# Performance work log

Measured on AMD Instinct MI355X. Metric: run time of the kernel, lower is better.

The kernel has to match this reference:

```python
import jax, jax.numpy as jnp
import numpy as np

D_MODEL = 1024
N_HEADS = 16
D_K = D_MODEL // N_HEADS
BATCH = 4
SEQ = 2048


def setup_inputs() -> dict:
    key = jax.random.key(0)
    ks = jax.random.split(key, 12)
    s = 1.0 / np.sqrt(D_MODEL)
    inp = {
        "context_sequence": jax.random.normal(ks[0], (BATCH, SEQ, D_MODEL), jnp.float32),
        "value_sequence": jax.random.normal(ks[1], (BATCH, SEQ, D_MODEL), jnp.float32),
        # True = masked (causal: cannot attend to future positions)
        "mask": jnp.triu(jnp.ones((SEQ, SEQ), dtype=bool), k=1),
        "Wq": jax.random.uniform(ks[2], (D_MODEL, D_MODEL), jnp.float32, -s, s),
        "bq": jax.random.uniform(ks[3], (D_MODEL,), jnp.float32, -s, s),
        "Wk": jax.random.uniform(ks[4], (D_MODEL, D_MODEL), jnp.float32, -s, s),
        "bk": jax.random.uniform(ks[5], (D_MODEL,), jnp.float32, -s, s),
        "Wv": jax.random.uniform(ks[6], (D_MODEL, D_MODEL), jnp.float32, -s, s),
        "bv": jax.random.uniform(ks[7], (D_MODEL,), jnp.float32, -s, s),
        "Wo": jax.random.uniform(ks[8], (D_MODEL, D_MODEL), jnp.float32, -s, s),
        "bo": jax.random.uniform(ks[9], (D_MODEL,), jnp.float32, -s, s),
    }
    return inp


def reference(context_sequence, value_sequence, mask, Wq, bq, Wk, bk, Wv, bv, Wo, bo):
    B, S, _ = context_sequence.shape
    # projections; split heads: [B, H, S, Dk]
    def split_heads(x):
        return x.reshape(B, S, N_HEADS, D_K).transpose(0, 2, 1, 3)

    Q = split_heads(context_sequence @ Wq + bq)
    K = split_heads(context_sequence @ Wk + bk)
    V = split_heads(value_sequence @ Wv + bv)

    scale = 1.0 / jnp.sqrt(jnp.asarray(D_K, dtype=Q.dtype))
    scores = jnp.einsum("bhqd,bhkd->bhqk", Q, K) * scale  # [B,H,S,S]
    scores = jnp.where(mask, jnp.asarray(-1e9, dtype=scores.dtype), scores)
    attn = jax.nn.softmax(scores, axis=-1)
    out = jnp.einsum("bhqk,bhkd->bhqd", attn, V)
    out = out.transpose(0, 2, 1, 3).reshape(B, S, D_MODEL)
    return out @ Wo + bo  # dropout p=0 (eval) -> identity
```

## Files before the change

kernel.cpp:

```cpp
#include <hip/hip_runtime.h>
#include <stdint.h>

#define D_MODEL 1024
#define SEQ 2048
#define BATCH 4
#define NH 16
#define DK 64

typedef float f32x4 __attribute__((ext_vector_type(4)));
typedef float f32x16 __attribute__((ext_vector_type(16)));
typedef __bf16 bf16x8 __attribute__((ext_vector_type(8)));
typedef unsigned short us4v __attribute__((ext_vector_type(4)));

__device__ __forceinline__ unsigned short f2bf(float f) {
  union { float f; unsigned u; } x; x.f = f;
  unsigned r = x.u + 0x7FFFu + ((x.u >> 16) & 1u);
  return (unsigned short)(r >> 16);
}

__device__ __forceinline__ void gll16(const void* g, void* l) {
  __builtin_amdgcn_global_load_lds(
      (__attribute__((address_space(1))) void*)g,
      (__attribute__((address_space(3))) void*)l, 16, 0, 0);
}

__device__ __forceinline__ int cvtpk(float lo, float hi) {
  int r;
  asm("v_cvt_pk_bf16_f32 %0, %1, %2" : "=v"(r) : "v"(lo), "v"(hi));
  return r;
}
__device__ __forceinline__ void pl32swap(int& a, int& b) {
  asm volatile("v_permlane32_swap_b32 %0, %1" : "+v"(a), "+v"(b));
}
__device__ __forceinline__ float exp2fast(float x) {
  float r;
  asm("v_exp_f32 %0, %1" : "=v"(r) : "v"(x));
  return r;
}

__global__ void cvtbf2(const float* __restrict__ a, const float* __restrict__ b,
                       unsigned short* __restrict__ out, const int nseg) {
  const int t = blockIdx.x * blockDim.x + threadIdx.x;
  const int stride = gridDim.x * blockDim.x;
  for (int i = t * 4; i < 2 * nseg; i += stride * 4) {
    const float* src = (i < nseg) ? &a[i] : &b[i - nseg];
    const float4 v = *(const float4*)src;
    us4v o;
    o[0] = f2bf(v.x); o[1] = f2bf(v.y); o[2] = f2bf(v.z); o[3] = f2bf(v.w);
    *(us4v*)&out[i] = o;
  }
}

__global__ void wtrans(const float* __restrict__ W0, const float* __restrict__ W1,
                       const float* __restrict__ W2, const float* __restrict__ W3,
                       unsigned short* __restrict__ T0, unsigned short* __restrict__ T1,
                       unsigned short* __restrict__ T2, unsigned short* __restrict__ T3) {
  __shared__ float t[32][33];
  const int z = blockIdx.z;
  const float* W = (z == 0) ? W0 : (z == 1) ? W1 : (z == 2) ? W2 : W3;
  unsigned short* T = (z == 0) ? T0 : (z == 1) ? T1 : (z == 2) ? T2 : T3;
  const int n0 = blockIdx.x * 32, k0 = blockIdx.y * 32;
  const int tx = threadIdx.x, ty = threadIdx.y;
#pragma unroll
  for (int i = 0; i < 4; ++i)
    t[ty + 8 * i][tx] = W[(size_t)(k0 + ty + 8 * i) * D_MODEL + n0 + tx];
  __syncthreads();
#pragma unroll
  for (int i = 0; i < 4; ++i)
    T[(size_t)(n0 + ty + 8 * i) * D_MODEL + k0 + tx] = f2bf(t[tx][ty + 8 * i]);
}

__global__ __launch_bounds__(256) void gemm128(
    const unsigned short* __restrict__ A, const unsigned short* __restrict__ Bt,
    const float* __restrict__ bias, unsigned short* __restrict__ outb,
    float* __restrict__ outf, const int mode) {
  __shared__ __align__(16) unsigned short Alds[2 * 128 * 64];
  __shared__ __align__(16) unsigned short Blds[2 * 128 * 64];
  const int tid = threadIdx.x;
  const int lane = tid & 63;
  const int w = tid >> 6;
  const int wr = w >> 1, wc = w & 1;

  int flat = (int)blockIdx.x + 8 * (int)blockIdx.y;
  flat = (flat & 7) * 64 + (flat >> 3);
  const int n0 = (flat & 7) * 128;
  const int m0 = (flat >> 3) * 128;

  const int srow = tid >> 3, sslot = tid & 7;

  auto stage = [&](int kk, int buf) {
#pragma unroll
    for (int i = 0; i < 4; ++i) {
      const int r = srow + 32 * i;
      const int gc = kk * 64 + ((sslot ^ (r & 7)) << 3);
      gll16(A + (size_t)(m0 + r) * D_MODEL + gc, &Alds[buf * 8192 + tid * 8 + i * 2048]);
      gll16(Bt + (size_t)(n0 + r) * D_MODEL + gc, &Blds[buf * 8192 + tid * 8 + i * 2048]);
    }
  };

  f32x4 acc[4][4] = {};

  stage(0, 0);
  stage(1, 1);

  const int NK = D_MODEL / 64;
  for (int kk = 0; kk < NK; ++kk) {
    const int cur = kk & 1;
    if (kk + 1 < NK) asm volatile("s_waitcnt vmcnt(8)" ::: "memory");
    else             asm volatile("s_waitcnt vmcnt(0)" ::: "memory");
    __builtin_amdgcn_s_barrier();
    asm volatile("" ::: "memory");

    const unsigned short* Al = &Alds[cur * 8192];
    const unsigned short* Bl = &Blds[cur * 8192];
#pragma unroll
    for (int kf = 0; kf < 2; ++kf) {
      const int sb = kf * 4 + (lane >> 4);
      bf16x8 a[4], b[4];
#pragma unroll
      for (int m = 0; m < 4; ++m) {
        const int row = wr * 64 + m * 16 + (lane & 15);
        a[m] = *(const bf16x8*)&Al[row * 64 + ((sb ^ (row & 7)) << 3)];
      }
#pragma unroll
      for (int n = 0; n < 4; ++n) {
        const int row = wc * 64 + n * 16 + (lane & 15);
        b[n] = *(const bf16x8*)&Bl[row * 64 + ((sb ^ (row & 7)) << 3)];
      }
#pragma unroll
      for (int m = 0; m < 4; ++m)
#pragma unroll
        for (int n = 0; n < 4; ++n)
          acc[m][n] = __builtin_amdgcn_mfma_f32_16x16x32_bf16(a[m], b[n], acc[m][n], 0, 0, 0);
    }

    asm volatile("" ::: "memory");
    __builtin_amdgcn_s_barrier();

    if (kk + 2 < NK) stage(kk + 2, cur);
  }

#pragma unroll
  for (int m = 0; m < 4; ++m) {
    const int rb = m0 + wr * 64 + m * 16 + ((lane >> 4) << 2);
#pragma unroll
    for (int n = 0; n < 4; ++n) {
      const int col = n0 + wc * 64 + n * 16 + (lane & 15);
      const float bv = bias[col];
#pragma unroll
      for (int j = 0; j < 4; ++j) {
        const int row = rb + j;
        const float v = acc[m][n][j] + bv;
        if (mode == 2) {
          outf[(size_t)row * D_MODEL + col] = v;
        } else {
          const int b_ = row >> 11, s_ = row & (SEQ - 1);
          const int h_ = col >> 6, d_ = col & (DK - 1);
          size_t idx;
          if (mode == 0) idx = (((size_t)(b_ * NH + h_)) * SEQ + s_) * DK + d_;
          else           idx = (((size_t)(b_ * NH + h_)) * DK + d_) * SEQ + s_;
          outb[idx] = f2bf(v);
        }
      }
    }
  }
}

__global__ __launch_bounds__(256, 4) void attn4w(
    const unsigned short* __restrict__ Q, const unsigned short* __restrict__ K,
    const unsigned short* __restrict__ Vt, unsigned short* __restrict__ O) {
  __shared__ __align__(16) unsigned short Klds[2 * 64 * 64];
  __shared__ __align__(16) unsigned short Vlds[2 * 64 * 64];

  const int tid = threadIdx.x, lane = tid & 63, w = tid >> 6;
  const int lq = lane & 31, hi = lane >> 5;
  const int bh = blockIdx.x;
  const int strip = 15 - (int)blockIdx.y;
  const size_t qkbase = (size_t)bh * SEQ * DK;
  const size_t vbase = (size_t)bh * DK * SEQ;
  const int srow = tid >> 3, sslot = tid & 7;
  const int b_ = bh >> 4, h_ = bh & (NH - 1);

  const int q0 = strip * 128;
  const int qw0 = q0 + w * 32;
  const int qg = qw0 + lq;
  const int n = 2 * strip + 2;

  bf16x8 qb[4];
  {
    const float QSCALE = 0.125f * 1.44269504f;
    const unsigned short* qp = Q + qkbase + (size_t)qg * DK + hi * 8;
#pragma unroll
    for (int ks = 0; ks < 4; ++ks) {
      qb[ks] = *(const bf16x8*)(qp + ks * 16);
#pragma unroll
      for (int e = 0; e < 8; ++e)
        qb[ks][e] = (__bf16)((float)qb[ks][e] * QSCALE);
    }
  }

  float m = -3e38f, l = 0.f;
  f32x16 o0 = {}, o1 = {};

#pragma unroll
  for (int i = 0; i < 2; ++i) {
    const int r = srow + 32 * i;
    const int sc = (sslot ^ (r & 7)) << 3;
    gll16(K + qkbase + (size_t)r * DK + sc, &Klds[tid * 8 + i * 2048]);
    gll16(Vt + vbase + (size_t)r * SEQ + sc, &Vlds[tid * 8 + i * 2048]);
  }
#pragma unroll
  for (int i = 0; i < 2; ++i) {
    const int r = srow + 32 * i;
    const int sc = (sslot ^ (r & 7)) << 3;
    gll16(K + qkbase + (size_t)(64 + r) * DK + sc, &Klds[4096 + tid * 8 + i * 2048]);
    gll16(Vt + vbase + (size_t)r * SEQ + 64 + sc, &Vlds[4096 + tid * 8 + i * 2048]);
  }

  for (int jt = 0; jt < n; ++jt) {
    const int cur = jt & 1;
    if (jt + 1 < n) asm volatile("s_waitcnt vmcnt(4)" ::: "memory");
    else            asm volatile("s_waitcnt vmcnt(0)" ::: "memory");
    __builtin_amdgcn_s_barrier();
    asm volatile("" ::: "memory");

    if (64 * jt < qw0 + 32) {
      const unsigned short* Kl = &Klds[cur * 4096];
      const unsigned short* Vl = &Vlds[cur * 4096];

      f32x16 st0 = {}, st1 = {};
      __builtin_amdgcn_s_setprio(1);
#pragma unroll
      for (int ks = 0; ks < 4; ++ks) {
        const int so = ((ks * 2 + hi) ^ (lq & 7)) << 3;
        const bf16x8 ka0 = *(const bf16x8*)&Kl[lq * 64 + so];
        const bf16x8 ka1 = *(const bf16x8*)&Kl[(32 + lq) * 64 + so];
        st0 = __builtin_amdgcn_mfma_f32_32x32x16_bf16(ka0, qb[ks], st0, 0, 0, 0);
        st1 = __builtin_amdgcn_mfma_f32_32x32x16_bf16(ka1, qb[ks], st1, 0, 0, 0);
      }
      __builtin_amdgcn_s_setprio(0);

      if (64 * jt + 63 > qw0) {
        const int rb = 64 * jt + 4 * hi - qg;
#pragma unroll
        for (int r = 0; r < 16; ++r) {
          const int crow0 = (r & 3) + 8 * (r >> 2);
          if (crow0 + rb > 0)      st0[r] = -3e38f;
          if (crow0 + 32 + rb > 0) st1[r] = -3e38f;
        }
      }

      float tmax[8];
#pragma unroll
      for (int r = 0; r < 8; ++r)
        tmax[r] = fmaxf(fmaxf(st0[r], st0[r + 8]), fmaxf(st1[r], st1[r + 8]));
      float mx = fmaxf(fmaxf(fmaxf(tmax[0], tmax[1]), fmaxf(tmax[2], tmax[3])),
                       fmaxf(fmaxf(tmax[4], tmax[5]), fmaxf(tmax[6], tmax[7])));
      mx = fmaxf(mx, __shfl_xor(mx, 32));

      if (__any((int)(mx > m + 11.5416f))) {
        const float mnew = fmaxf(m, mx);
        const float alpha = exp2fast(m - mnew);
        m = mnew;
        l *= alpha;
#pragma unroll
        for (int r = 0; r < 16; ++r) { o0[r] *= alpha; o1[r] *= alpha; }
      }

#pragma unroll
      for (int r = 0; r < 16; ++r) {
        st0[r] = exp2fast(st0[r] - m);
        st1[r] = exp2fast(st1[r] - m);
      }

      float tsum[8];
#pragma unroll
      for (int r = 0; r < 8; ++r)
        tsum[r] = (st0[r] + st0[r + 8]) + (st1[r] + st1[r + 8]);
      float rs = ((tsum[0] + tsum[1]) + (tsum[2] + tsum[3])) +
                 ((tsum[4] + tsum[5]) + (tsum[6] + tsum[7]));
      rs += __shfl_xor(rs, 32);
      l += rs;

      bf16x8 pb[4];
#pragma unroll
      for (int ks = 0; ks < 4; ++ks) {
        const int base = (ks & 1) * 8;
        float p0, p1, p2, p3, p4, p5, p6, p7;
        if (ks < 2) {
          p0 = st0[base + 0]; p1 = st0[base + 1]; p2 = st0[base + 2]; p3 = st0[base + 3];
          p4 = st0[base + 4]; p5 = st0[base + 5]; p6 = st0[base + 6]; p7 = st0[base + 7];
        } else {
          p0 = st1[base + 0]; p1 = st1[base + 1]; p2 = st1[base + 2]; p3 = st1[base + 3];
          p4 = st1[base + 4]; p5 = st1[base + 5]; p6 = st1[base + 6]; p7 = st1[base + 7];
        }
        int a0 = cvtpk(p0, p1), a1 = cvtpk(p2, p3);
        int a2 = cvtpk(p4, p5), a3 = cvtpk(p6, p7);
        pl32swap(a0, a2);
        pl32swap(a1, a3);
        union { int i[4]; bf16x8 v; } u;
        u.i[0] = a0; u.i[1] = a1; u.i[2] = a2; u.i[3] = a3;
        pb[ks] = u.v;
      }

      __builtin_amdgcn_s_setprio(1);
#pragma unroll
      for (int ks = 0; ks < 4; ++ks) {
        const int so = ((ks * 2 + hi) ^ (lq & 7)) << 3;
        const bf16x8 va0 = *(const bf16x8*)&Vl[lq * 64 + so];
        const bf16x8 va1 = *(const bf16x8*)&Vl[(32 + lq) * 64 + so];
        o0 = __builtin_amdgcn_mfma_f32_32x32x16_bf16(va0, pb[ks], o0, 0, 0, 0);
        o1 = __builtin_amdgcn_mfma_f32_32x32x16_bf16(va1, pb[ks], o1, 0, 0, 0);
      }
      __builtin_amdgcn_s_setprio(0);
    }

    asm volatile("" ::: "memory");
    __builtin_amdgcn_s_barrier();

    if (jt + 2 < n) {
      const int kv0 = (jt + 2) * 64;
#pragma unroll
      for (int i = 0; i < 2; ++i) {
        const int r = srow + 32 * i;
        const int sc = (sslot ^ (r & 7)) << 3;
        gll16(K + qkbase + (size_t)(kv0 + r) * DK + sc,
              &Klds[cur * 4096 + tid * 8 + i * 2048]);
        gll16(Vt + vbase + (size_t)r * SEQ + kv0 + sc,
              &Vlds[cur * 4096 + tid * 8 + i * 2048]);
      }
    }
  }

  const float rl = 1.0f / l;
  unsigned short* orow = O + (size_t)(b_ * SEQ + qg) * D_MODEL + h_ * DK;
#pragma unroll
  for (int g = 0; g < 4; ++g) {
    us4v pk0, pk1;
#pragma unroll
    for (int j = 0; j < 4; ++j) {
      pk0[j] = f2bf(o0[4 * g + j] * rl);
      pk1[j] = f2bf(o1[4 * g + j] * rl);
    }
    const int d0 = 8 * g + 4 * hi;
    *(us4v*)&orow[d0] = pk0;
    *(us4v*)&orow[32 + d0] = pk1;
  }
}

extern "C" void kernel_launch(void* const* d_in, const int* in_sizes, int n_in,
                              void* d_out, int out_size, void* d_ws, size_t ws_size,
                              hipStream_t stream) {
  const float* ctx = (const float*)d_in[0];
  const float* val = (const float*)d_in[1];
  const float* Wq = (const float*)d_in[3];
  const float* bq = (const float*)d_in[4];
  const float* Wk = (const float*)d_in[5];
  const float* bk = (const float*)d_in[6];
  const float* Wv = (const float*)d_in[7];
  const float* bv = (const float*)d_in[8];
  const float* Wo = (const float*)d_in[9];
  const float* bo = (const float*)d_in[10];

  unsigned short* ws = (unsigned short*)d_ws;
  const size_t XSZ = (size_t)BATCH * SEQ * D_MODEL;
  const size_t WSZ = (size_t)D_MODEL * D_MODEL;
  unsigned short* Xc  = ws;
  unsigned short* Xv  = Xc + XSZ;
  unsigned short* Wqt = Xv + XSZ;
  unsigned short* Wkt = Wqt + WSZ;
  unsigned short* Wvt = Wkt + WSZ;
  unsigned short* Wot = Wvt + WSZ;
  unsigned short* Qb  = Wot + WSZ;
  unsigned short* Kb  = Qb + XSZ;
  unsigned short* Vtb = Kb + XSZ;
  unsigned short* Ob  = Vtb + XSZ;

  cvtbf2<<<2048, 256, 0, stream>>>(ctx, val, Xc, (int)XSZ);
  wtrans<<<dim3(32, 32, 4), dim3(32, 8), 0, stream>>>(Wq, Wk, Wv, Wo, Wqt, Wkt, Wvt, Wot);

  dim3 gg(D_MODEL / 128, BATCH * SEQ / 128);
  gemm128<<<gg, 256, 0, stream>>>(Xc, Wqt, bq, Qb, nullptr, 0);
  gemm128<<<gg, 256, 0, stream>>>(Xc, Wkt, bk, Kb, nullptr, 0);
  gemm128<<<gg, 256, 0, stream>>>(Xv, Wvt, bv, Vtb, nullptr, 1);

  attn4w<<<dim3(BATCH * NH, 16), 256, 0, stream>>>(Qb, Kb, Vtb, Ob);

  gemm128<<<gg, 256, 0, stream>>>(Ob, Wot, bo, nullptr, (float*)d_out, 2);
}
```

Before: 180.1 us.

## Batch QKV GEMMs into one launch and triple-buffer attention K/V loads

The three Q/K/V projection GEMMs become one launch using blockIdx.z to pick operands, which removes two launches and lets their tails overlap. In the attention kernel, K/V staging moves to a three-slot LDS ring issued right after the barrier, so the second barrier per iteration is dropped and prefetch starts earlier. The row-sum cross-half shuffle is deferred to after the loop, and the max reduction now uses permlane32_swap instead of a shuffle. Occupancy hint drops from 4 to 3 blocks per CU because LDS use grows by half.

```diff
diff --git a/kernel.cpp b/kernel.cpp
--- a/kernel.cpp
+++ b/kernel.cpp
@@ -31,6 +31,12 @@
 }
 __device__ __forceinline__ void pl32swap(int& a, int& b) {
   asm volatile("v_permlane32_swap_b32 %0, %1" : "+v"(a), "+v"(b));
+}
+__device__ __forceinline__ float xmax32(float x) {
+  int a = __float_as_int(x), b;
+  asm volatile("v_mov_b32 %0, %1" : "=v"(b) : "v"(a));
+  pl32swap(a, b);
+  return fmaxf(__int_as_float(a), __int_as_float(b));
 }
 __device__ __forceinline__ float exp2fast(float x) {
   float r;
@@ -70,12 +76,11 @@
     T[(size_t)(n0 + ty + 8 * i) * D_MODEL + k0 + tx] = f2bf(t[tx][ty + 8 * i]);
 }
 
-__global__ __launch_bounds__(256) void gemm128(
+__device__ __forceinline__ void gemm_body(
     const unsigned short* __restrict__ A, const unsigned short* __restrict__ Bt,
     const float* __restrict__ bias, unsigned short* __restrict__ outb,
-    float* __restrict__ outf, const int mode) {
-  __shared__ __align__(16) unsigned short Alds[2 * 128 * 64];
-  __shared__ __align__(16) unsigned short Blds[2 * 128 * 64];
+    float* __restrict__ outf, const int mode,
+    unsigned short* Alds, unsigned short* Blds) {
   const int tid = threadIdx.x;
   const int lane = tid & 63;
   const int w = tid >> 6;
@@ -166,11 +171,37 @@
   }
 }
 
-__global__ __launch_bounds__(256, 4) void attn4w(
+__global__ __launch_bounds__(256) void gemmQKV(
+    const unsigned short* __restrict__ Xc, const unsigned short* __restrict__ Xv,
+    const unsigned short* __restrict__ Wqt, const unsigned short* __restrict__ Wkt,
+    const unsigned short* __restrict__ Wvt,
+    const float* __restrict__ bq, const float* __restrict__ bk,
+    const float* __restrict__ bv,
+    unsigned short* __restrict__ Qb, unsigned short* __restrict__ Kb,
+    unsigned short* __restrict__ Vtb) {
+  __shared__ __align__(16) unsigned short Alds[2 * 128 * 64];
+  __shared__ __align__(16) unsigned short Blds[2 * 128 * 64];
+  const int z = blockIdx.z;
+  const unsigned short* A = (z == 2) ? Xv : Xc;
+  const unsigned short* Bt = (z == 0) ? Wqt : (z == 1) ? Wkt : Wvt;
+  const float* bias = (z == 0) ? bq : (z == 1) ? bk : bv;
+  unsigned short* outb = (z == 0) ? Qb : (z == 1) ? Kb : Vtb;
+  gemm_body(A, Bt, bias, outb, nullptr, (z == 2) ? 1 : 0, Alds, Blds);
+}
+
+__global__ __launch_bounds__(256) void gemmO(
+    const unsigned short* __restrict__ A, const unsigned short* __restrict__ Bt,
+    const float* __restrict__ bias, float* __restrict__ outf) {
+  __shared__ __align__(16) unsigned short Alds[2 * 128 * 64];
+  __shared__ __align__(16) unsigned short Blds[2 * 128 * 64];
+  gemm_body(A, Bt, bias, nullptr, outf, 2, Alds, Blds);
+}
+
+__global__ __launch_bounds__(256, 3) void attn4w(
     const unsigned short* __restrict__ Q, const unsigned short* __restrict__ K,
     const unsigned short* __restrict__ Vt, unsigned short* __restrict__ O) {
-  __shared__ __align__(16) unsigned short Klds[2 * 64 * 64];
-  __shared__ __align__(16) unsigned short Vlds[2 * 64 * 64];
+  __shared__ __align__(16) unsigned short Klds[3 * 64 * 64];
+  __shared__ __align__(16) unsigned short Vlds[3 * 64 * 64];
 
   const int tid = threadIdx.x, lane = tid & 63, w = tid >> 6;
   const int lq = lane & 31, hi = lane >> 5;
@@ -186,6 +217,18 @@
   const int qg = qw0 + lq;
   const int n = 2 * strip + 2;
 
+  auto stageKV = [&](int t, int slot) {
+#pragma unroll
+    for (int i = 0; i < 2; ++i) {
+      const int r = srow + 32 * i;
+      const int sc = (sslot ^ (r & 7)) << 3;
+      gll16(K + qkbase + (size_t)(t * 64 + r) * DK + sc,
+            &Klds[slot * 4096 + tid * 8 + i * 2048]);
+      gll16(Vt + vbase + (size_t)r * SEQ + t * 64 + sc,
+            &Vlds[slot * 4096 + tid * 8 + i * 2048]);
+    }
+  };
+
   bf16x8 qb[4];
   {
     const float QSCALE = 0.125f * 1.44269504f;
@@ -202,31 +245,21 @@
   float m = -3e38f, l = 0.f;
   f32x16 o0 = {}, o1 = {};
 
-#pragma unroll
-  for (int i = 0; i < 2; ++i) {
-    const int r = srow + 32 * i;
-    const int sc = (sslot ^ (r & 7)) << 3;
-    gll16(K + qkbase + (size_t)r * DK + sc, &Klds[tid * 8 + i * 2048]);
-    gll16(Vt + vbase + (size_t)r * SEQ + sc, &Vlds[tid * 8 + i * 2048]);
-  }
-#pragma unroll
-  for (int i = 0; i < 2; ++i) {
-    const int r = srow + 32 * i;
-    const int sc = (sslot ^ (r & 7)) << 3;
-    gll16(K + qkbase + (size_t)(64 + r) * DK + sc, &Klds[4096 + tid * 8 + i * 2048]);
-    gll16(Vt + vbase + (size_t)r * SEQ + 64 + sc, &Vlds[4096 + tid * 8 + i * 2048]);
-  }
+  stageKV(0, 0);
+  stageKV(1, 1);
 
   for (int jt = 0; jt < n; ++jt) {
-    const int cur = jt & 1;
+    const int slot = jt % 3;
     if (jt + 1 < n) asm volatile("s_waitcnt vmcnt(4)" ::: "memory");
     else            asm volatile("s_waitcnt vmcnt(0)" ::: "memory");
     __builtin_amdgcn_s_barrier();
     asm volatile("" ::: "memory");
 
+    if (jt + 2 < n) stageKV(jt + 2, (jt + 2) % 3);
+
     if (64 * jt < qw0 + 32) {
-      const unsigned short* Kl = &Klds[cur * 4096];
-      const unsigned short* Vl = &Vlds[cur * 4096];
+      const unsigned short* Kl = &Klds[slot * 4096];
+      const unsigned short* Vl = &Vlds[slot * 4096];
 
       f32x16 st0 = {}, st1 = {};
       __builtin_amdgcn_s_setprio(1);
@@ -256,7 +289,7 @@
         tmax[r] = fmaxf(fmaxf(st0[r], st0[r + 8]), fmaxf(st1[r], st1[r + 8]));
       float mx = fmaxf(fmaxf(fmaxf(tmax[0], tmax[1]), fmaxf(tmax[2], tmax[3])),
                        fmaxf(fmaxf(tmax[4], tmax[5]), fmaxf(tmax[6], tmax[7])));
-      mx = fmaxf(mx, __shfl_xor(mx, 32));
+      mx = xmax32(mx);
 
       if (__any((int)(mx > m + 11.5416f))) {
         const float mnew = fmaxf(m, mx);
@@ -277,10 +310,8 @@
 #pragma unroll
       for (int r = 0; r < 8; ++r)
         tsum[r] = (st0[r] + st0[r + 8]) + (st1[r] + st1[r + 8]);
-      float rs = ((tsum[0] + tsum[1]) + (tsum[2] + tsum[3])) +
-                 ((tsum[4] + tsum[5]) + (tsum[6] + tsum[7]));
-      rs += __shfl_xor(rs, 32);
-      l += rs;
+      l += ((tsum[0] + tsum[1]) + (tsum[2] + tsum[3])) +
+           ((tsum[4] + tsum[5]) + (tsum[6] + tsum[7]));
 
       bf16x8 pb[4];
 #pragma unroll
@@ -314,24 +345,10 @@
       }
       __builtin_amdgcn_s_setprio(0);
     }
-
     asm volatile("" ::: "memory");
-    __builtin_amdgcn_s_barrier();
-
-    if (jt + 2 < n) {
-      const int kv0 = (jt + 2) * 64;
-#pragma unroll
-      for (int i = 0; i < 2; ++i) {
-        const int r = srow + 32 * i;
-        const int sc = (sslot ^ (r & 7)) << 3;
-        gll16(K + qkbase + (size_t)(kv0 + r) * DK + sc,
-              &Klds[cur * 4096 + tid * 8 + i * 2048]);
-        gll16(Vt + vbase + (size_t)r * SEQ + kv0 + sc,
-              &Vlds[cur * 4096 + tid * 8 + i * 2048]);
-      }
-    }
-  }
-
+  }
+
+  l += __shfl_xor(l, 32);
   const float rl = 1.0f / l;
   unsigned short* orow = O + (size_t)(b_ * SEQ + qg) * D_MODEL + h_ * DK;
 #pragma unroll
@@ -379,12 +396,10 @@
   cvtbf2<<<2048, 256, 0, stream>>>(ctx, val, Xc, (int)XSZ);
   wtrans<<<dim3(32, 32, 4), dim3(32, 8), 0, stream>>>(Wq, Wk, Wv, Wo, Wqt, Wkt, Wvt, Wot);
 
-  dim3 gg(D_MODEL / 128, BATCH * SEQ / 128);
-  gemm128<<<gg, 256, 0, stream>>>(Xc, Wqt, bq, Qb, nullptr, 0);
-  gemm128<<<gg, 256, 0, stream>>>(Xc, Wkt, bk, Kb, nullptr, 0);
-  gemm128<<<gg, 256, 0, stream>>>(Xv, Wvt, bv, Vtb, nullptr, 1);
+  gemmQKV<<<dim3(8, 64, 3), 256, 0, stream>>>(Xc, Xv, Wqt, Wkt, Wvt,
+                                              bq, bk, bv, Qb, Kb, Vtb);
 
   attn4w<<<dim3(BATCH * NH, 16), 256, 0, stream>>>(Qb, Kb, Vtb, Ob);
 
-  gemm128<<<gg, 256, 0, stream>>>(Ob, Wot, bo, nullptr, (float*)d_out, 2);
-}
+  gemmO<<<dim3(8, 64), 256, 0, stream>>>(Ob, Wot, bo, (float*)d_out);
+}
```

Result: faster. 169.9 us (-5.7%).
